# Performance work log

Measured on AMD Instinct MI355X. Metric: run time of the kernel, lower is better.

Reference implementation:

```python
import jax, jax.numpy as jnp
import numpy as np

B, N, DIM, H = 4, 8192, 1024, 16
HD = DIM // H
DFF = 4 * DIM
EPS_LN = 1e-5
EPS_NORM = 1e-6


def _layernorm(x, w, b):
    mu = jnp.mean(x, axis=-1, keepdims=True)
    var = jnp.mean(jnp.square(x - mu), axis=-1, keepdims=True)
    return (x - mu) * jax.lax.rsqrt(var + EPS_LN) * w + b


def _phi(x):
    # elu feature map: elu(x) + 1
    return jax.nn.elu(x) + 1.0


def setup_inputs() -> dict:
    key = jax.random.key(0)
    ks = jax.random.split(key, 8)
    s = 0.02
    return {
        "src": jax.random.normal(ks[0], (B, N, DIM), jnp.float32),
        "ln1_w": jnp.ones((DIM,), jnp.float32),
        "ln1_b": jnp.zeros((DIM,), jnp.float32),
        "wq": jax.random.normal(ks[1], (DIM, DIM), jnp.float32) * s,
        "wk": jax.random.normal(ks[2], (DIM, DIM), jnp.float32) * s,
        "wv": jax.random.normal(ks[3], (DIM, DIM), jnp.float32) * s,
        "wo": jax.random.normal(ks[4], (DIM, DIM), jnp.float32) * s,
        "ln2_w": jnp.ones((DIM,), jnp.float32),
        "ln2_b": jnp.zeros((DIM,), jnp.float32),
        "fc1_w": jax.random.normal(ks[5], (DIM, DFF), jnp.float32) * s,
        "fc1_b": jnp.zeros((DFF,), jnp.float32),
        "fc2_w": jax.random.normal(ks[6], (DFF, DIM), jnp.float32) * s,
        "fc2_b": jnp.zeros((DIM,), jnp.float32),
    }


def _linear_attention(x, wq, wk, wv, wo):
    # x: [B, N, DIM]; self-attention (query=key=value=x)
    q = (x @ wq).reshape(B, N, H, HD).transpose(0, 2, 1, 3)  # bhnd
    k = (x @ wk).reshape(B, N, H, HD).transpose(0, 2, 1, 3)
    v = (x @ wv).reshape(B, N, H, HD).transpose(0, 2, 1, 3)
    q = _phi(q)
    k = _phi(k)
    kv = jnp.einsum('bhsd,bhse->bhde', k, v)        # [B,H,HD,HD]
    out = jnp.einsum('bhqd,bhde->bhqe', q, kv)      # [B,H,N,HD]
    k_sum = jnp.sum(k, axis=2)                      # [B,H,HD]
    normalizer = jnp.einsum('bhqd,bhd->bhq', q, k_sum)[..., None] + EPS_NORM
    out = out / normalizer
    out = out.transpose(0, 2, 1, 3).reshape(B, N, DIM)
    return out @ wo


def reference(src, ln1_w, ln1_b, wq, wk, wv, wo, ln2_w, ln2_b, fc1_w, fc1_b, fc2_w, fc2_b):
    # forward_pre: pre-norm transformer block with linear (elu) attention
    h = _layernorm(src, ln1_w, ln1_b)
    src = src + _linear_attention(h, wq, wk, wv, wo)
    h = _layernorm(src, ln2_w, ln2_b)
    h = jax.nn.gelu(h @ fc1_w + fc1_b, approximate=False)  # torch nn.GELU exact
    src = src + (h @ fc2_w + fc2_b)
    return src
```

## Files before the change

kernel.cpp:

```cpp
#include <hip/hip_runtime.h>
#include <hip/hip_bf16.h>

typedef __attribute__((ext_vector_type(8))) short s16x8;
typedef __attribute__((ext_vector_type(4))) short s16x4;
typedef __attribute__((ext_vector_type(8))) __bf16 bf16x8;
typedef __attribute__((ext_vector_type(4))) float f32x4;

__device__ __forceinline__ float b2f(short s) {
  union { float f; unsigned u; } x;
  x.u = ((unsigned)(unsigned short)s) << 16;
  return x.f;
}
__device__ __forceinline__ short f2b(float f) {
  union { float f; unsigned u; } x;
  x.f = f;
  unsigned r = x.u + 0x7fff + ((x.u >> 16) & 1);
  return (short)(r >> 16);
}
__device__ __forceinline__ bf16x8 asbf(s16x8 v) {
  union { s16x8 s; bf16x8 b; } u; u.s = v; return u.b;
}

#define GLD16(g, l) __builtin_amdgcn_global_load_lds( \
    (const __attribute__((address_space(1))) void*)(g), \
    (__attribute__((address_space(3))) void*)(l), 16, 0, 0)

#define WAITB4 do { \
  asm volatile("s_waitcnt vmcnt(4)" ::: "memory"); \
  __builtin_amdgcn_s_barrier(); \
  asm volatile("" ::: "memory"); \
} while (0)

__global__ __launch_bounds__(256) void transpose_cvt(
    const float* __restrict__ in, short* __restrict__ out, int R, int C) {
  __shared__ float tile[32][33];
  const int tx = threadIdx.x & 31, ty = threadIdx.x >> 5;
  const int c0 = blockIdx.x * 32, r0 = blockIdx.y * 32;
  #pragma unroll
  for (int i = 0; i < 32; i += 8)
    tile[ty + i][tx] = in[(size_t)(r0 + ty + i) * C + c0 + tx];
  __syncthreads();
  #pragma unroll
  for (int i = 0; i < 32; i += 8)
    out[(size_t)(c0 + ty + i) * R + r0 + tx] = f2b(tile[tx][ty + i]);
}

__global__ __launch_bounds__(256) void ln_kernel(
    const float* __restrict__ x, const float* __restrict__ gw,
    const float* __restrict__ gb, short* __restrict__ out) {
  const int row = blockIdx.x;
  const int tid = threadIdx.x;
  const float4 v = ((const float4*)(x + (size_t)row * 1024))[tid];
  float s = v.x + v.y + v.z + v.w;
  float s2 = v.x * v.x + v.y * v.y + v.z * v.z + v.w * v.w;
  #pragma unroll
  for (int o = 32; o > 0; o >>= 1) {
    s += __shfl_xor(s, o);
    s2 += __shfl_xor(s2, o);
  }
  __shared__ float red[2][4];
  const int lane = tid & 63, wid = tid >> 6;
  if (lane == 0) { red[0][wid] = s; red[1][wid] = s2; }
  __syncthreads();
  s = red[0][0] + red[0][1] + red[0][2] + red[0][3];
  s2 = red[1][0] + red[1][1] + red[1][2] + red[1][3];
  const float mu = s * (1.f / 1024.f);
  const float rstd = rsqrtf(s2 * (1.f / 1024.f) - mu * mu + 1e-5f);
  const float4 wv4 = ((const float4*)gw)[tid];
  const float4 bv4 = ((const float4*)gb)[tid];
  s16x4 o4;
  o4.x = f2b((v.x - mu) * rstd * wv4.x + bv4.x);
  o4.y = f2b((v.y - mu) * rstd * wv4.y + bv4.y);
  o4.z = f2b((v.z - mu) * rstd * wv4.z + bv4.z);
  o4.w = f2b((v.w - mu) * rstd * wv4.w + bv4.w);
  *(s16x4*)(out + (size_t)row * 1024 + tid * 4) = o4;
}


enum { EPI_QKV = 0, EPI_RES = 1, EPI_GELU = 2, EPI_FC2 = 3 };

#define PHASE(BUFB, MH, KS, LOADB) do { \
    const int ab = (BUFB) + (KS) * 16384; \
    const int bb = (BUFB) + 32768 + (KS) * 16384; \
    if (LOADB) { \
      _Pragma("unroll") \
      for (int n = 0; n < 4; n++) { \
        const int row = wnCol + n * 16 + fr; \
        const int g = row >> 1; \
        const int s = (((row & 1) << 2) | fq) ^ (g & 7); \
        bfv[n] = *(const bf16x8*)(ldsc + bb + g * 128 + s * 16); \
      } \
    } \
    bf16x8 af[4]; \
    _Pragma("unroll") \
    for (int mm = 0; mm < 4; mm++) { \
      const int row = wmRow + (MH) * 64 + mm * 16 + fr; \
      const int g = row >> 1; \
      const int s = (((row & 1) << 2) | fq) ^ (g & 7); \
      af[mm] = *(const bf16x8*)(ldsc + ab + g * 128 + s * 16); \
    } \
    __builtin_amdgcn_s_setprio(1); \
    _Pragma("unroll") \
    for (int mm = 0; mm < 4; mm++) \
      _Pragma("unroll") \
      for (int n = 0; n < 4; n++) \
        acc[(MH) * 4 + mm][n] = __builtin_amdgcn_mfma_f32_16x16x32_bf16( \
            af[mm], bfv[n], acc[(MH) * 4 + mm][n], 0, 0, 0); \
    __builtin_amdgcn_s_setprio(0); \
  } while (0)

template <int EPI>
__global__ __launch_bounds__(512, 2) void gemm256(
    const short* __restrict__ A, int lda,
    const short* __restrict__ Bt, int K, int ldo, int gx,
    const float* __restrict__ bias,
    const float* __restrict__ resid,
    void* __restrict__ outp) {
  __shared__ alignas(16) short lds[65536];
  const int tid = threadIdx.x;
  const int lane = tid & 63, wave = tid >> 6;
  const int cpx = (int)gridDim.x >> 3;
  const int bid = ((int)blockIdx.x & 7) * cpx + ((int)blockIdx.x >> 3);
  const int bm = (bid % gx) * 256;
  const int bn = (bid / gx) * 256;
  const int wmRow = (wave >> 2) * 128;
  const int wnCol = (wave & 3) * 64;
  const int fr = lane & 15, fq = lane >> 4;

  const int sg = tid >> 3;
  const int s0 = (tid & 7) ^ (sg & 7);
  const int srow = 2 * sg + (s0 >> 2);
  const int scol = (s0 & 3) * 8;
  const int sdst = tid * 16;

  const char* ldsc = (const char*)lds;
  char* ldsw = (char*)lds;

  f32x4 acc[8][4] = {};
  bf16x8 bfv[4];

  auto stageA = [&](int bufb, int kh, int kk) {
    const short* g = A + (size_t)(bm + srow) * lda + kk + kh * 32 + scol;
    char* l = ldsw + bufb + kh * 16384 + sdst;
    GLD16(g, l);
    GLD16(g + (size_t)128 * lda, l + 8192);
  };
  auto stageB = [&](int bufb, int kh, int kk) {
    const short* g = Bt + (size_t)(bn + srow) * K + kk + kh * 32 + scol;
    char* l = ldsw + bufb + 32768 + kh * 16384 + sdst;
    GLD16(g, l);
    GLD16(g + (size_t)128 * K, l + 8192);
  };

  const int NT = K >> 6;
  stageA(0, 0, 0);
  stageB(0, 0, 0);
  stageA(0, 1, 0);
  stageB(0, 1, 0);
  WAITB4;

  int buf = 0;
  for (int t = 0; t < NT; ++t) {
    const int kkn = (t + 1 < NT) ? ((t + 1) << 6) : 0;
    const int nb = buf ^ 65536;
    stageA(nb, 0, kkn);
    PHASE(buf, 0, 0, true);
    stageB(nb, 0, kkn);
    PHASE(buf, 1, 0, false);
    WAITB4;
    stageA(nb, 1, kkn);
    PHASE(buf, 0, 1, true);
    stageB(nb, 1, kkn);
    PHASE(buf, 1, 1, false);
    WAITB4;
    buf = nb;
  }
  asm volatile("s_waitcnt vmcnt(0)" ::: "memory");

  const int row0 = bm + wmRow + fq * 4;
  const int col0 = bn + wnCol + fr;
  #pragma unroll
  for (int m = 0; m < 8; m++) {
    #pragma unroll
    for (int n = 0; n < 4; n++) {
      const int col = col0 + n * 16;
      #pragma unroll
      for (int r = 0; r < 4; r++) {
        const int row = row0 + m * 16 + r;
        float v = acc[m][n][r];
        if constexpr (EPI == EPI_QKV) {
          if (col < 2048) v = (v > 0.f) ? (v + 1.f) : __expf(v);
          ((short*)outp)[(size_t)row * ldo + col] = f2b(v);
        } else if constexpr (EPI == EPI_RES) {
          ((float*)outp)[(size_t)row * ldo + col] =
              v + resid[(size_t)row * ldo + col];
        } else if constexpr (EPI == EPI_GELU) {
          v += bias[col];
          v = 0.5f * v * (1.f + erff(v * 0.70710678118654752f));
          ((short*)outp)[(size_t)row * ldo + col] = f2b(v);
        } else {
          v += bias[col] + resid[(size_t)row * ldo + col];
          ((float*)outp)[(size_t)row * ldo + col] = v;
        }
      }
    }
  }
}

__global__ __launch_bounds__(256) void kv_reduce(
    const short* __restrict__ qkv, float* __restrict__ kv_part,
    float* __restrict__ ksum_part) {
  const int blk = blockIdx.x;
  const int bh = blk >> 5, chunk = blk & 31;
  const int b = bh >> 4, h = bh & 15;
  const size_t rowbase = (size_t)b * 8192 + (size_t)chunk * 256;
  const int kcol = 1024 + h * 64, vcol = 2048 + h * 64;
  __shared__ short Kl[64][64];
  __shared__ short Vl[64][64];
  const int tid = threadIdx.x;
  const int dk = tid >> 2, dq = tid & 3;
  float acc[16] = {};
  float ks = 0.f;
  for (int t = 0; t < 4; t++) {
    #pragma unroll
    for (int i = 0; i < 2; i++) {
      const int s = i * 256 + tid;
      const int r = s >> 3, seg = (s & 7) * 8;
      const size_t g = (rowbase + t * 64 + r) * 3072;
      *(s16x8*)&Kl[r][seg] = *(const s16x8*)&qkv[g + kcol + seg];
      *(s16x8*)&Vl[r][seg] = *(const s16x8*)&qkv[g + vcol + seg];
    }
    __syncthreads();
    for (int n = 0; n < 64; n++) {
      const float kval = b2f(Kl[n][dk]);
      if (dq == 0) ks += kval;
      const s16x8 v0 = *(const s16x8*)&Vl[n][dq * 16];
      const s16x8 v1 = *(const s16x8*)&Vl[n][dq * 16 + 8];
      #pragma unroll
      for (int j = 0; j < 8; j++) {
        acc[j] = fmaf(kval, b2f(v0[j]), acc[j]);
        acc[8 + j] = fmaf(kval, b2f(v1[j]), acc[8 + j]);
      }
    }
    __syncthreads();
  }
  float* dst = kv_part + (size_t)blk * 4096 + dk * 64 + dq * 16;
  #pragma unroll
  for (int j = 0; j < 16; j++) dst[j] = acc[j];
  if (dq == 0) ksum_part[(size_t)blk * 64 + dk] = ks;
}

__global__ __launch_bounds__(256) void kv_finalize(
    const float* __restrict__ kv_part, const float* __restrict__ ksum_part,
    short* __restrict__ kvT_g, float* __restrict__ ksum_f) {
  const int bh = blockIdx.x >> 2, dg = blockIdx.x & 3;
  const int tid = threadIdx.x;
  const int e = tid & 63, j4 = tid >> 6;
  const int d0 = dg * 16 + j4 * 4;
  float a0 = 0.f, a1 = 0.f, a2 = 0.f, a3 = 0.f;
  const float* base = kv_part + (size_t)bh * 32 * 4096 + d0 * 64 + e;
  for (int c = 0; c < 32; c++) {
    const float* p = base + (size_t)c * 4096;
    a0 += p[0]; a1 += p[64]; a2 += p[128]; a3 += p[192];
  }
  s16x4 o; o.x = f2b(a0); o.y = f2b(a1); o.z = f2b(a2); o.w = f2b(a3);
  char* dstb = (char*)(kvT_g + (size_t)bh * 4096);
  *(s16x4*)(dstb + e * 128 + ((2 * d0) ^ ((e & 7) << 4))) = o;
  if (tid < 16) {
    const int d = dg * 16 + tid;
    float s = 0.f;
    for (int c = 0; c < 32; c++)
      s += ksum_part[((size_t)bh * 32 + c) * 64 + d];
    ksum_f[bh * 64 + d] = s;
  }
}

__global__ __launch_bounds__(256) void attn_apply_mfma(
    const short* __restrict__ qkv, const short* __restrict__ kvT_g,
    const float* __restrict__ ksum_f, short* __restrict__ ao) {
  __shared__ alignas(16) short kvs[4096];
  __shared__ float ksl[64];
  const int blk = blockIdx.x;
  const int bh = blk >> 5, rc = blk & 31;
  const int b = bh >> 4, h = bh & 15;
  const int tid = threadIdx.x, lane = tid & 63, w = tid >> 6;
  const int fr = lane & 15, fq = lane >> 4;

  GLD16(kvT_g + (size_t)bh * 4096 + tid * 8, (char*)kvs + tid * 16);
  GLD16(kvT_g + (size_t)bh * 4096 + (256 + tid) * 8, (char*)kvs + (256 + tid) * 16);
  if (tid < 64) ksl[tid] = ksum_f[bh * 64 + tid];
  __syncthreads();

  bf16x8 bkv[4][2], bns[2];
  #pragma unroll
  for (int n = 0; n < 4; n++) {
    #pragma unroll
    for (int c = 0; c < 2; c++) {
      const int e = n * 16 + fr;
      const int byteoff = e * 128 + ((c * 64 + fq * 16) ^ ((e & 7) << 4));
      bkv[n][c] = *(const bf16x8*)((const char*)kvs + byteoff);
    }
  }
  #pragma unroll
  for (int c = 0; c < 2; c++) {
    s16x8 ts = {0, 0, 0, 0, 0, 0, 0, 0};
    if (fr == 0) {
      #pragma unroll
      for (int j = 0; j < 8; j++) ts[j] = f2b(ksl[c * 32 + fq * 8 + j]);
    }
    bns[c] = asbf(ts);
  }

  f32x4 acc[4][4] = {};
  f32x4 nacc[4] = {};
  const size_t rowbase = (size_t)b * 8192 + (size_t)rc * 256 + w * 64;
  const int qcol = h * 64;
  #pragma unroll
  for (int m = 0; m < 4; m++) {
    const short* qrow = qkv + (rowbase + m * 16 + fr) * 3072 + qcol + fq * 8;
    const bf16x8 a0 = *(const bf16x8*)qrow;
    const bf16x8 a1 = *(const bf16x8*)(qrow + 32);
    #pragma unroll
    for (int n = 0; n < 4; n++) {
      acc[m][n] = __builtin_amdgcn_mfma_f32_16x16x32_bf16(a0, bkv[n][0], acc[m][n], 0, 0, 0);
      acc[m][n] = __builtin_amdgcn_mfma_f32_16x16x32_bf16(a1, bkv[n][1], acc[m][n], 0, 0, 0);
    }
    nacc[m] = __builtin_amdgcn_mfma_f32_16x16x32_bf16(a0, bns[0], nacc[m], 0, 0, 0);
    nacc[m] = __builtin_amdgcn_mfma_f32_16x16x32_bf16(a1, bns[1], nacc[m], 0, 0, 0);
  }

  #pragma unroll
  for (int m = 0; m < 4; m++) {
    #pragma unroll
    for (int r = 0; r < 4; r++) {
      const float nv = __shfl(nacc[m][r], lane & 48) + 1e-6f;
      const float rn = 1.f / nv;
      const size_t row = rowbase + m * 16 + fq * 4 + r;
      #pragma unroll
      for (int n = 0; n < 4; n++)
        ao[row * 1024 + qcol + n * 16 + fr] = f2b(acc[m][n][r] * rn);
    }
  }
}

extern "C" void kernel_launch(void* const* d_in, const int* in_sizes, int n_in,
                              void* d_out, int out_size, void* d_ws, size_t ws_size,
                              hipStream_t stream) {
  (void)in_sizes; (void)n_in; (void)out_size; (void)ws_size;
  const float* src   = (const float*)d_in[0];
  const float* ln1_w = (const float*)d_in[1];
  const float* ln1_b = (const float*)d_in[2];
  const float* wq    = (const float*)d_in[3];
  const float* wk    = (const float*)d_in[4];
  const float* wv    = (const float*)d_in[5];
  const float* wo    = (const float*)d_in[6];
  const float* ln2_w = (const float*)d_in[7];
  const float* ln2_b = (const float*)d_in[8];
  const float* fc1_w = (const float*)d_in[9];
  const float* fc1_b = (const float*)d_in[10];
  const float* fc2_w = (const float*)d_in[11];
  const float* fc2_b = (const float*)d_in[12];

  char* ws = (char*)d_ws;
  short* wqkvT     = (short*)(ws + 0);
  short* woT       = (short*)(ws + 6291456);
  short* fc1T      = (short*)(ws + 8388608);
  short* fc2T      = (short*)(ws + 16777216);
  short* kvT_g     = (short*)(ws + 25165824);
  float* ksum_f    = (float*)(ws + 25690112);
  float* kv_part   = (float*)(ws + 25706496);
  float* ksum_part = (float*)(ws + 59260928);
  short* hbuf      = (short*)(ws + 59785216);
  float* src2      = (float*)(ws + 126894080);
  short* qkv       = (short*)(ws + 261111808);
  short* a1c       = (short*)(ws + 261111808);

  const dim3 tb(256);
  const dim3 tb512(512);

  transpose_cvt<<<dim3(32, 32), tb, 0, stream>>>(wq, wqkvT, 1024, 1024);
  transpose_cvt<<<dim3(32, 32), tb, 0, stream>>>(wk, wqkvT + 1024 * 1024, 1024, 1024);
  transpose_cvt<<<dim3(32, 32), tb, 0, stream>>>(wv, wqkvT + 2048 * 1024, 1024, 1024);
  transpose_cvt<<<dim3(32, 32), tb, 0, stream>>>(wo, woT, 1024, 1024);
  transpose_cvt<<<dim3(128, 32), tb, 0, stream>>>(fc1_w, fc1T, 1024, 4096);
  transpose_cvt<<<dim3(32, 128), tb, 0, stream>>>(fc2_w, fc2T, 4096, 1024);

  ln_kernel<<<32768, tb, 0, stream>>>(src, ln1_w, ln1_b, hbuf);

  gemm256<EPI_QKV><<<dim3(1536), tb512, 0, stream>>>(
      hbuf, 1024, wqkvT, 1024, 3072, 128, nullptr, nullptr, qkv);

  kv_reduce<<<2048, tb, 0, stream>>>(qkv, kv_part, ksum_part);
  kv_finalize<<<256, tb, 0, stream>>>(kv_part, ksum_part, kvT_g, ksum_f);

  attn_apply_mfma<<<2048, tb, 0, stream>>>(qkv, kvT_g, ksum_f, hbuf);

  gemm256<EPI_RES><<<dim3(512), tb512, 0, stream>>>(
      hbuf, 1024, woT, 1024, 1024, 128, nullptr, src, src2);

  ln_kernel<<<32768, tb, 0, stream>>>(src2, ln2_w, ln2_b, hbuf);

  for (int c = 0; c < 2; c++) {
    const size_t mo = (size_t)c * 16384;
    gemm256<EPI_GELU><<<dim3(1024), tb512, 0, stream>>>(
        hbuf + mo * 1024, 1024, fc1T, 1024, 4096, 64, fc1_b, nullptr, a1c);
    gemm256<EPI_FC2><<<dim3(256), tb512, 0, stream>>>(
        a1c, 4096, fc2T, 4096, 1024, 64, fc2_b, src2 + mo * 1024,
        (float*)d_out + mo * 1024);
  }
}
```

Baseline: 1.271 ms.

## Restructure GEMM main loop into barrier-delimited LDS-read and MFMA phases

Splits the GEMM inner phase into separate LDS fragment reads, global-to-LDS stage issue and a 16-MFMA block. Each MFMA block is bracketed by workgroup barriers, with an lgkmcnt(0) wait before it and the vmcnt wait moved ahead of the pre-MFMA barrier. This aims to keep waves in lockstep, a ping-pong style schedule, so that LDS reads and memory issue of some waves overlap the matrix-core work of others. In exchange it adds four barriers per half-iteration, which may cost more than the overlap gains if the waves do not interleave well.

```diff
diff --git a/kernel.cpp b/kernel.cpp
--- a/kernel.cpp
+++ b/kernel.cpp
@@ -24,12 +24,6 @@
 #define GLD16(g, l) __builtin_amdgcn_global_load_lds( \
     (const __attribute__((address_space(1))) void*)(g), \
     (__attribute__((address_space(3))) void*)(l), 16, 0, 0)
-
-#define WAITB4 do { \
-  asm volatile("s_waitcnt vmcnt(4)" ::: "memory"); \
-  __builtin_amdgcn_s_barrier(); \
-  asm volatile("" ::: "memory"); \
-} while (0)
 
 __global__ __launch_bounds__(256) void transpose_cvt(
     const float* __restrict__ in, short* __restrict__ out, int R, int C) {
@@ -79,26 +73,27 @@
 
 enum { EPI_QKV = 0, EPI_RES = 1, EPI_GELU = 2, EPI_FC2 = 3 };
 
-#define PHASE(BUFB, MH, KS, LOADB) do { \
-    const int ab = (BUFB) + (KS) * 16384; \
-    const int bb = (BUFB) + 32768 + (KS) * 16384; \
-    if (LOADB) { \
-      _Pragma("unroll") \
-      for (int n = 0; n < 4; n++) { \
-        const int row = wnCol + n * 16 + fr; \
-        const int g = row >> 1; \
-        const int s = (((row & 1) << 2) | fq) ^ (g & 7); \
-        bfv[n] = *(const bf16x8*)(ldsc + bb + g * 128 + s * 16); \
-      } \
+#define READB(BUFB, KS) do { \
+    _Pragma("unroll") \
+    for (int n = 0; n < 4; n++) { \
+      const int row = wnCol + n * 16 + fr; \
+      const int g = row >> 1; \
+      const int s = (((row & 1) << 2) | fq) ^ (g & 7); \
+      bfv[n] = *(const bf16x8*)(ldsc + (BUFB) + 32768 + (KS) * 16384 + g * 128 + s * 16); \
     } \
-    bf16x8 af[4]; \
+  } while (0)
+
+#define READA(BUFB, MH, KS) do { \
     _Pragma("unroll") \
     for (int mm = 0; mm < 4; mm++) { \
       const int row = wmRow + (MH) * 64 + mm * 16 + fr; \
       const int g = row >> 1; \
       const int s = (((row & 1) << 2) | fq) ^ (g & 7); \
-      af[mm] = *(const bf16x8*)(ldsc + ab + g * 128 + s * 16); \
+      af[mm] = *(const bf16x8*)(ldsc + (BUFB) + (KS) * 16384 + g * 128 + s * 16); \
     } \
+  } while (0)
+
+#define MFMA16(MH) do { \
     __builtin_amdgcn_s_setprio(1); \
     _Pragma("unroll") \
     for (int mm = 0; mm < 4; mm++) \
@@ -108,6 +103,14 @@
             af[mm], bfv[n], acc[(MH) * 4 + mm][n], 0, 0, 0); \
     __builtin_amdgcn_s_setprio(0); \
   } while (0)
+
+#define PREBAR do { \
+    __builtin_amdgcn_s_barrier(); \
+    asm volatile("s_waitcnt lgkmcnt(0)" ::: "memory"); \
+  } while (0)
+
+#define VM4 asm volatile("s_waitcnt vmcnt(4)" ::: "memory")
+#define POSTBAR __builtin_amdgcn_s_barrier()
 
 template <int EPI>
 __global__ __launch_bounds__(512, 2) void gemm256(
@@ -137,7 +140,7 @@
   char* ldsw = (char*)lds;
 
   f32x4 acc[8][4] = {};
-  bf16x8 bfv[4];
+  bf16x8 af[4], bfv[4];
 
   auto stageA = [&](int bufb, int kh, int kk) {
     const short* g = A + (size_t)(bm + srow) * lda + kk + kh * 32 + scol;
@@ -157,22 +160,37 @@
   stageB(0, 0, 0);
   stageA(0, 1, 0);
   stageB(0, 1, 0);
-  WAITB4;
+  VM4;
+  __builtin_amdgcn_s_barrier();
 
   int buf = 0;
   for (int t = 0; t < NT; ++t) {
     const int kkn = (t + 1 < NT) ? ((t + 1) << 6) : 0;
     const int nb = buf ^ 65536;
+    READB(buf, 0);
+    READA(buf, 0, 0);
     stageA(nb, 0, kkn);
-    PHASE(buf, 0, 0, true);
+    PREBAR;
+    MFMA16(0);
+    POSTBAR;
+    READA(buf, 1, 0);
     stageB(nb, 0, kkn);
-    PHASE(buf, 1, 0, false);
-    WAITB4;
+    VM4;
+    PREBAR;
+    MFMA16(1);
+    POSTBAR;
+    READB(buf, 1);
+    READA(buf, 0, 1);
     stageA(nb, 1, kkn);
-    PHASE(buf, 0, 1, true);
+    PREBAR;
+    MFMA16(0);
+    POSTBAR;
+    READA(buf, 1, 1);
     stageB(nb, 1, kkn);
-    PHASE(buf, 1, 1, false);
-    WAITB4;
+    VM4;
+    PREBAR;
+    MFMA16(1);
+    POSTBAR;
     buf = nb;
   }
   asm volatile("s_waitcnt vmcnt(0)" ::: "memory");
```

Result: slower. 1.325 ms (+4.3%).

## Double-buffer LDS fragment registers to overlap ds_reads with MFMA in GEMM loop

Applied to the files above, without the earlier changes.

Restructures the GEMM main loop so the A/B fragments for the next phase are read from LDS into a second register set while MFMAs run on the current set. Explicit lgkmcnt waits and sched_barriers pin the interleaving, and barriers are moved so the next tile's first fragments are prefetched right after the barrier. The aim is to hide LDS read latency behind matrix math. In exchange it costs extra VGPRs, which could hurt occupancy at launch_bounds(512,2), and the hand-counted waits are fragile.

```diff
diff --git a/kernel.cpp b/kernel.cpp
--- a/kernel.cpp
+++ b/kernel.cpp
@@ -25,11 +25,9 @@
     (const __attribute__((address_space(1))) void*)(g), \
     (__attribute__((address_space(3))) void*)(l), 16, 0, 0)
 
-#define WAITB4 do { \
-  asm volatile("s_waitcnt vmcnt(4)" ::: "memory"); \
-  __builtin_amdgcn_s_barrier(); \
-  asm volatile("" ::: "memory"); \
-} while (0)
+#define VMW(N) asm volatile("s_waitcnt vmcnt(" #N ")" ::: "memory")
+#define LGKM(N) asm volatile("s_waitcnt lgkmcnt(" #N ")" ::: "memory")
+#define SCHED0 __builtin_amdgcn_sched_barrier(0)
 
 __global__ __launch_bounds__(256) void transpose_cvt(
     const float* __restrict__ in, short* __restrict__ out, int R, int C) {
@@ -79,33 +77,34 @@
 
 enum { EPI_QKV = 0, EPI_RES = 1, EPI_GELU = 2, EPI_FC2 = 3 };
 
-#define PHASE(BUFB, MH, KS, LOADB) do { \
-    const int ab = (BUFB) + (KS) * 16384; \
-    const int bb = (BUFB) + 32768 + (KS) * 16384; \
-    if (LOADB) { \
-      _Pragma("unroll") \
-      for (int n = 0; n < 4; n++) { \
-        const int row = wnCol + n * 16 + fr; \
-        const int g = row >> 1; \
-        const int s = (((row & 1) << 2) | fq) ^ (g & 7); \
-        bfv[n] = *(const bf16x8*)(ldsc + bb + g * 128 + s * 16); \
-      } \
-    } \
-    bf16x8 af[4]; \
+#define READ_AF(DST, BUFB, MH, KS) do { \
     _Pragma("unroll") \
     for (int mm = 0; mm < 4; mm++) { \
       const int row = wmRow + (MH) * 64 + mm * 16 + fr; \
       const int g = row >> 1; \
       const int s = (((row & 1) << 2) | fq) ^ (g & 7); \
-      af[mm] = *(const bf16x8*)(ldsc + ab + g * 128 + s * 16); \
+      DST[mm] = *(const bf16x8*)(ldsc + (BUFB) + (KS) * 16384 + g * 128 + s * 16); \
     } \
+  } while (0)
+
+#define READ_BFV(DST, BUFB, KS) do { \
+    _Pragma("unroll") \
+    for (int n = 0; n < 4; n++) { \
+      const int row = wnCol + n * 16 + fr; \
+      const int g = row >> 1; \
+      const int s = (((row & 1) << 2) | fq) ^ (g & 7); \
+      DST[n] = *(const bf16x8*)(ldsc + (BUFB) + 32768 + (KS) * 16384 + g * 128 + s * 16); \
+    } \
+  } while (0)
+
+#define MFMA16(AH, AF, BF) do { \
     __builtin_amdgcn_s_setprio(1); \
     _Pragma("unroll") \
     for (int mm = 0; mm < 4; mm++) \
       _Pragma("unroll") \
       for (int n = 0; n < 4; n++) \
-        acc[(MH) * 4 + mm][n] = __builtin_amdgcn_mfma_f32_16x16x32_bf16( \
-            af[mm], bfv[n], acc[(MH) * 4 + mm][n], 0, 0, 0); \
+        acc[(AH) * 4 + mm][n] = __builtin_amdgcn_mfma_f32_16x16x32_bf16( \
+            AF[mm], BF[n], acc[(AH) * 4 + mm][n], 0, 0, 0); \
     __builtin_amdgcn_s_setprio(0); \
   } while (0)
 
@@ -137,7 +136,7 @@
   char* ldsw = (char*)lds;
 
   f32x4 acc[8][4] = {};
-  bf16x8 bfv[4];
+  bf16x8 afA[4], afB[4], bfvA[4], bfvB[4];
 
   auto stageA = [&](int bufb, int kh, int kk) {
     const short* g = A + (size_t)(bm + srow) * lda + kk + kh * 32 + scol;
@@ -157,25 +156,44 @@
   stageB(0, 0, 0);
   stageA(0, 1, 0);
   stageB(0, 1, 0);
-  WAITB4;
+  VMW(4);
+  __builtin_amdgcn_s_barrier();
+  READ_BFV(bfvA, 0, 0);
+  READ_AF(afA, 0, 0, 0);
 
   int buf = 0;
   for (int t = 0; t < NT; ++t) {
     const int kkn = (t + 1 < NT) ? ((t + 1) << 6) : 0;
     const int nb = buf ^ 65536;
     stageA(nb, 0, kkn);
-    PHASE(buf, 0, 0, true);
+    READ_AF(afB, buf, 1, 0);
+    SCHED0;
+    LGKM(4);
+    MFMA16(0, afA, bfvA);
     stageB(nb, 0, kkn);
-    PHASE(buf, 1, 0, false);
-    WAITB4;
+    VMW(4);
+    __builtin_amdgcn_s_barrier();
+    READ_BFV(bfvB, buf, 1);
+    READ_AF(afA, buf, 0, 1);
+    SCHED0;
+    LGKM(8);
+    MFMA16(1, afB, bfvA);
     stageA(nb, 1, kkn);
-    PHASE(buf, 0, 1, true);
+    READ_AF(afB, buf, 1, 1);
+    SCHED0;
+    LGKM(4);
+    MFMA16(0, afA, bfvB);
     stageB(nb, 1, kkn);
-    PHASE(buf, 1, 1, false);
-    WAITB4;
+    LGKM(0);
+    VMW(4);
+    __builtin_amdgcn_s_barrier();
+    READ_BFV(bfvA, nb, 0);
+    READ_AF(afA, nb, 0, 0);
+    SCHED0;
+    MFMA16(1, afB, bfvB);
     buf = nb;
   }
-  asm volatile("s_waitcnt vmcnt(0)" ::: "memory");
+  VMW(0);
 
   const int row0 = bm + wmRow + fq * 4;
   const int col0 = bn + wnCol + fr;
```

Result: no change. 1.287 ms (+1.3%).
